# Kernel tuning notes

Measured on AMD Instinct MI355X. Metric: run time of the kernel, lower is better.

Reference implementation:

```python
import jax, jax.numpy as jnp
import numpy as np

N, S, E, H = 2, 2048, 1024, 16
D = E // H  # head_dim = 64


def setup_inputs() -> dict:
    key = jax.random.key(0)
    k1, k2, k3 = jax.random.split(key, 3)
    x = jax.random.normal(k1, (N, S, E), dtype=jnp.float32)
    # Xavier-uniform-scaled weights (torch Linear layout: [out_features, in_features])
    lim_qkv = (6.0 / (E + 3 * E)) ** 0.5
    qkv_w = jax.random.uniform(k2, (3 * E, E), dtype=jnp.float32, minval=-lim_qkv, maxval=lim_qkv)
    lim_o = (6.0 / (E + E)) ** 0.5
    o_w = jax.random.uniform(k3, (E, E), dtype=jnp.float32, minval=-lim_o, maxval=lim_o)
    # causal look-ahead mask: positions where mask == 0 are excluded
    attn_mask = jnp.tril(jnp.ones((S, S), dtype=jnp.int32))
    return {"x": x, "attn_mask": attn_mask, "qkv_w": qkv_w, "o_w": o_w}


def reference(x, attn_mask, qkv_w, o_w):
    n, s, e = x.shape
    qkv = x @ qkv_w.T                              # (N, S, 3E)
    q, k, v = jnp.split(qkv, 3, axis=-1)
    # (N, S, E) -> (N, H, S, D)
    def to_heads(t):
        return t.reshape(n, s, H, D).transpose(0, 2, 1, 3)
    q, k, v = to_heads(q), to_heads(k), to_heads(v)
    scale = 1.0 / jnp.sqrt(jnp.asarray(D, dtype=x.dtype))
    logits = jnp.einsum('bhqd,bhkd->bhqk', q, k) * scale   # (N, H, S, S)
    mask = attn_mask.reshape(1, 1, s, s)                    # expand_mask: 2D -> (1,1,S,S)
    logits = jnp.where(mask == 0, -jnp.inf, logits)
    attn_weights = jax.nn.softmax(logits, axis=-1)
    values = jnp.einsum('bhqk,bhkd->bhqd', attn_weights, v)  # (N, H, S, D)
    values = values.transpose(0, 2, 1, 3).reshape(n, s, e)
    o = values @ o_w.T
    return o
```

## Files before the change

### kernel.cpp

```cpp
#include <hip/hip_runtime.h>
#include <math.h>

typedef unsigned short u16;
typedef unsigned int uint;
typedef __attribute__((ext_vector_type(8))) short bf16x8;
typedef __attribute__((ext_vector_type(8))) _Float16 half8;
typedef __attribute__((ext_vector_type(4))) float floatx4;

__device__ __forceinline__ u16 f2bf(float f) {
  union { float f; uint u; } c; c.f = f;
  return (u16)((c.u + 0x7FFFu + ((c.u >> 16) & 1u)) >> 16);
}
__device__ __forceinline__ float bf2f(u16 h) {
  union { uint u; float f; } c; c.u = ((uint)h) << 16;
  return c.f;
}
__device__ __forceinline__ u16 h2u(_Float16 h) {
  union { _Float16 h; u16 u; } c; c.h = h;
  return c.u;
}

#if __has_builtin(__builtin_amdgcn_exp2f)
#define EX2 __builtin_amdgcn_exp2f
#else
#define EX2 exp2f
#endif

__device__ __forceinline__ void gl_lds16(const u16* g, u16* l) {
  __builtin_amdgcn_global_load_lds(
      (const __attribute__((address_space(1))) uint*)g,
      (__attribute__((address_space(3))) uint*)l, 16, 0, 0);
}

__device__ __forceinline__ void store_c(u16* p, float v) { *p = f2bf(v); }
__device__ __forceinline__ void store_c(float* p, float v) { *p = v; }

#define ROR16(x, n)                                                        \
  __builtin_bit_cast(float, __builtin_amdgcn_update_dpp(                   \
      __builtin_bit_cast(int, (x)), __builtin_bit_cast(int, (x)),          \
      0x120 + (n), 0xF, 0xF, false))
__device__ __forceinline__ float rsum16(float x) {
  x += ROR16(x, 8); x += ROR16(x, 4); x += ROR16(x, 2); x += ROR16(x, 1);
  return x;
}

__global__ __launch_bounds__(256) void cvt_all(const float* __restrict__ x,
                                               const float* __restrict__ qw,
                                               const float* __restrict__ ow,
                                               u16* __restrict__ xb,
                                               u16* __restrict__ wb,
                                               u16* __restrict__ ob) {
  int bx = blockIdx.x;
  const float* src; u16* dst; int off;
  if (bx < 2048) { src = x; dst = xb; off = bx; }
  else if (bx < 3584) { src = qw; dst = wb; off = bx - 2048; }
  else { src = ow; dst = ob; off = bx - 3584; }
  int i = (off * 256 + threadIdx.x) * 8;
  float4 a = *(const float4*)(src + i);
  float4 b = *(const float4*)(src + i + 4);
  bf16x8 r;
  r[0] = (short)f2bf(a.x); r[1] = (short)f2bf(a.y);
  r[2] = (short)f2bf(a.z); r[3] = (short)f2bf(a.w);
  r[4] = (short)f2bf(b.x); r[5] = (short)f2bf(b.y);
  r[6] = (short)f2bf(b.z); r[7] = (short)f2bf(b.w);
  *(bf16x8*)(dst + i) = r;
}

__global__ __launch_bounds__(256) void vtrans(const u16* __restrict__ qkv,
                                              u16* __restrict__ vt) {
  constexpr int S = 2048, E = 1024, TE = 3072;
  __shared__ u16 tile[64 * 72];
  const int t = threadIdx.x;
  const int kv0 = blockIdx.x * 64;
  const int bh = blockIdx.y, b = bh >> 4, h = bh & 15;
  const u16* src = qkv + (size_t)b * S * TE + 2 * E + h * 64;
#pragma unroll
  for (int i = 0; i < 2; ++i) {
    int c = t + i * 256;
    int kv = c >> 3, d0 = (c & 7) * 8;
    *(bf16x8*)&tile[kv * 72 + d0] = *(const bf16x8*)&src[(size_t)(kv0 + kv) * TE + d0];
  }
  __syncthreads();
  u16* dst = vt + (size_t)bh * 64 * S + kv0;
#pragma unroll
  for (int i = 0; i < 2; ++i) {
    int c = t + i * 256;
    int d = c >> 3, k0 = (c & 7) * 8;
    bf16x8 r;
#pragma unroll
    for (int j = 0; j < 8; ++j)
      r[j] = (short)h2u((_Float16)bf2f(tile[(k0 + j) * 72 + d]));
    *(bf16x8*)&dst[(size_t)d * S + k0] = r;
  }
}

template <typename TC>
__global__ __launch_bounds__(256) void gemm_bt(const u16* __restrict__ A,
                                               const u16* __restrict__ B,
                                               TC* __restrict__ C,
                                               int K, int N) {
  __shared__ __align__(16) u16 lds_a[128 * 64];
  __shared__ __align__(16) u16 lds_b[128 * 64];
  const int t = threadIdx.x;
  const int w = t >> 6, lane = t & 63, quad = lane >> 4, lr = lane & 15;
  const int wr = w >> 1, wc = w & 1;
  const int m0 = blockIdx.y * 128, n0 = blockIdx.x * 128;

  const int srow = lane >> 3;
  const int scol = ((lane & 7) ^ srow) * 8;
  const u16* Ab = A + (size_t)(m0 + w * 32 + srow) * K + scol;
  const u16* Bb = B + (size_t)(n0 + w * 32 + srow) * K + scol;
  u16* la = lds_a + (w * 32) * 64;
  u16* lb = lds_b + (w * 32) * 64;

  floatx4 acc[4][4];
#pragma unroll
  for (int i = 0; i < 4; ++i)
#pragma unroll
    for (int j = 0; j < 4; ++j) acc[i][j] = {0.f, 0.f, 0.f, 0.f};

  for (int k0 = 0; k0 < K; k0 += 64) {
#pragma unroll
    for (int j = 0; j < 4; ++j) {
      gl_lds16(Ab + (size_t)(j * 8) * K + k0, la + j * 8 * 64);
      gl_lds16(Bb + (size_t)(j * 8) * K + k0, lb + j * 8 * 64);
    }
    __syncthreads();
#pragma unroll
    for (int kk = 0; kk < 2; ++kk) {
      bf16x8 af[4], bfr[4];
#pragma unroll
      for (int mi = 0; mi < 4; ++mi)
        af[mi] = *(const bf16x8*)&lds_a[(wr * 64 + mi * 16 + lr) * 64 +
                                        (((kk * 4 + quad) ^ (lr & 7)) * 8)];
#pragma unroll
      for (int ni = 0; ni < 4; ++ni)
        bfr[ni] = *(const bf16x8*)&lds_b[(wc * 64 + ni * 16 + lr) * 64 +
                                         (((kk * 4 + quad) ^ (lr & 7)) * 8)];
#pragma unroll
      for (int mi = 0; mi < 4; ++mi)
#pragma unroll
        for (int ni = 0; ni < 4; ++ni)
          acc[mi][ni] = __builtin_amdgcn_mfma_f32_16x16x32_bf16(
              af[mi], bfr[ni], acc[mi][ni], 0, 0, 0);
    }
    __syncthreads();
  }
#pragma unroll
  for (int mi = 0; mi < 4; ++mi)
#pragma unroll
    for (int r = 0; r < 4; ++r) {
      int m = m0 + wr * 64 + mi * 16 + quad * 4 + r;
#pragma unroll
      for (int ni = 0; ni < 4; ++ni) {
        int n = n0 + wc * 64 + ni * 16 + lr;
        store_c(&C[(size_t)m * N + n], acc[mi][ni][r]);
      }
    }
}

template <typename TC>
__global__ __launch_bounds__(256) void gemm_bt64(const u16* __restrict__ A,
                                                 const u16* __restrict__ B,
                                                 TC* __restrict__ C,
                                                 int K, int N) {
  __shared__ __align__(16) u16 lds_a[64 * 64];
  __shared__ __align__(16) u16 lds_b[128 * 64];
  const int t = threadIdx.x;
  const int w = t >> 6, lane = t & 63, quad = lane >> 4, lr = lane & 15;
  const int m0 = blockIdx.y * 64, n0 = blockIdx.x * 128;

  const int srow = lane >> 3;
  const int scol = ((lane & 7) ^ srow) * 8;
  const u16* Ab = A + (size_t)(m0 + srow) * K + scol;
  const u16* Bb = B + (size_t)(n0 + srow) * K + scol;

  floatx4 acc[4][2];
#pragma unroll
  for (int i = 0; i < 4; ++i)
#pragma unroll
    for (int j = 0; j < 2; ++j) acc[i][j] = {0.f, 0.f, 0.f, 0.f};

  for (int k0 = 0; k0 < K; k0 += 64) {
#pragma unroll
    for (int i = 0; i < 2; ++i)
      gl_lds16(Ab + (size_t)((w * 2 + i) * 8) * K + k0, &lds_a[(w * 2 + i) * 8 * 64]);
#pragma unroll
    for (int i = 0; i < 4; ++i)
      gl_lds16(Bb + (size_t)((w * 4 + i) * 8) * K + k0, &lds_b[(w * 4 + i) * 8 * 64]);
    __syncthreads();
#pragma unroll
    for (int kk = 0; kk < 2; ++kk) {
      bf16x8 af[4], bfr[2];
#pragma unroll
      for (int mi = 0; mi < 4; ++mi)
        af[mi] = *(const bf16x8*)&lds_a[(mi * 16 + lr) * 64 +
                                        (((kk * 4 + quad) ^ (lr & 7)) * 8)];
#pragma unroll
      for (int ni = 0; ni < 2; ++ni)
        bfr[ni] = *(const bf16x8*)&lds_b[(w * 32 + ni * 16 + lr) * 64 +
                                         (((kk * 4 + quad) ^ (lr & 7)) * 8)];
#pragma unroll
      for (int mi = 0; mi < 4; ++mi)
#pragma unroll
        for (int ni = 0; ni < 2; ++ni)
          acc[mi][ni] = __builtin_amdgcn_mfma_f32_16x16x32_bf16(
              af[mi], bfr[ni], acc[mi][ni], 0, 0, 0);
    }
    __syncthreads();
  }
#pragma unroll
  for (int mi = 0; mi < 4; ++mi)
#pragma unroll
    for (int r = 0; r < 4; ++r) {
      int m = m0 + mi * 16 + quad * 4 + r;
#pragma unroll
      for (int ni = 0; ni < 2; ++ni) {
        int n = n0 + w * 32 + ni * 16 + lr;
        store_c(&C[(size_t)m * N + n], acc[mi][ni][r]);
      }
    }
}

__global__ __launch_bounds__(512, 2) void attn_fwd(const u16* __restrict__ qkv,
                                                   const u16* __restrict__ vt,
                                                   u16* __restrict__ out,
                                                   float* __restrict__ opart,
                                                   float* __restrict__ lpart) {
  constexpr int S = 2048, E = 1024, TE = 3072;
  constexpr float NEG = -1e30f;
  __shared__ __align__(16) u16 lds_k[2][128 * 64];
  __shared__ __align__(16) u16 lds_vt[2][64 * 128];
  __shared__ __align__(16) u16 lds_p[2][4][16 * 128];
  const int t = threadIdx.x;
  const int wv = t >> 6;
  const int u = wv >> 2;
  const int w = wv & 3;
  const int lane = t & 63, quad = lane >> 4, lr = lane & 15;
  const int bx = (int)blockIdx.x;
  const int h = bx & 15, pr = (bx >> 4) & 7, hB = bx >> 7;
  const int qtH = 15 - pr;
  const int b = u;
  const int bh = b * 16 + h;
  const int pid = (b * 16 + h) * 8 + pr;
  const size_t base = (size_t)b * S * TE;
  const u16* kbase = qkv + base + E + h * 64;
  const u16* vtb = vt + (size_t)bh * 64 * S;

  const int s8 = lane >> 3;
  const int kcol = ((lane & 7) ^ s8) * 8;
  const int vrow = lane >> 4;
  u16* const pb = &lds_p[u][w][0];
  u16* const lk = &lds_k[u][0];
  u16* const lv = &lds_vt[u][0];

  const int n0 = hB ? (8 - pr) : 8;
  const int niter = hB ? 9 : 8;

  const float QS = 0.125f * 1.44269504f;
  bf16x8 qf[2][2];
  float lst[2][4];
  floatx4 oacc[2][4];

  auto load_q = [&](int qt) {
#pragma unroll
    for (int rg = 0; rg < 2; ++rg)
#pragma unroll
      for (int kk = 0; kk < 2; ++kk) {
        bf16x8 q = *(const bf16x8*)&qkv[base +
            (size_t)(qt * 128 + w * 32 + rg * 16 + lr) * TE + h * 64 + kk * 32 + quad * 8];
#pragma unroll
        for (int jj = 0; jj < 8; ++jj) q[jj] = (short)f2bf(bf2f((u16)q[jj]) * QS);
        qf[rg][kk] = q;
      }
  };
  auto reset_acc = [&]() {
#pragma unroll
    for (int rg = 0; rg < 2; ++rg) {
#pragma unroll
      for (int r = 0; r < 4; ++r) lst[rg][r] = 0.f;
#pragma unroll
      for (int di = 0; di < 4; ++di) oacc[rg][di] = {0.f, 0.f, 0.f, 0.f};
    }
  };
  auto emit_partial = [&](int slot) {
    float* op = opart + ((size_t)slot * 256 + pid) * (128 * 64);
    float* lp = lpart + ((size_t)slot * 256 + pid) * 128;
#pragma unroll
    for (int rg = 0; rg < 2; ++rg)
#pragma unroll
      for (int r = 0; r < 4; ++r) {
        int row = w * 32 + rg * 16 + quad * 4 + r;
        float lt = rsum16(lst[rg][r]);
        if (lr == 0) lp[row] = lt;
#pragma unroll
        for (int di = 0; di < 4; ++di)
          op[row * 64 + di * 16 + lr] = oacc[rg][di][r];
      }
  };
  auto kv_of = [&](int it) -> int {
    if (!hB) return it;
    return (it < n0) ? (8 + it) : (it - n0);
  };

  load_q(qtH);
  reset_acc();

  {
    int nb = kv_of(0) * 128;
#pragma unroll
    for (int i = 0; i < 4; ++i) {
      int p0 = w * 8 + i * 32;
      int kv = nb + ((p0 & 15) + s8) * 8 + (p0 >> 4);
      gl_lds16(kbase + (size_t)kv * TE + kcol, &lk[p0 * 64]);
    }
#pragma unroll
    for (int i = 0; i < 4; ++i) {
      int d0 = w * 4 + i * 16;
      int d = d0 + vrow;
      int cbg = ((lane & 15) ^ (d & 15)) * 8;
      gl_lds16(vtb + (size_t)d * S + nb + cbg, &lv[d0 * 128]);
    }
  }

  for (int it = 0; it < niter; ++it) {
    const int kt = kv_of(it);
    const int qcur = (hB && it >= n0) ? pr : qtH;
    __syncthreads();

    floatx4 st[2][8];
#pragma unroll
    for (int rg = 0; rg < 2; ++rg)
#pragma unroll
      for (int ni = 0; ni < 8; ++ni) st[rg][ni] = {-4.f, -4.f, -4.f, -4.f};
#pragma unroll
    for (int kk = 0; kk < 2; ++kk) {
      bf16x8 kb[8];
#pragma unroll
      for (int ni = 0; ni < 8; ++ni)
        kb[ni] = *(const bf16x8*)&lk[(ni * 16 + lr) * 64 +
                                     (((kk * 4 + quad) ^ (lr & 7)) * 8)];
#pragma unroll
      for (int rg = 0; rg < 2; ++rg)
#pragma unroll
        for (int ni = 0; ni < 8; ++ni)
          st[rg][ni] = __builtin_amdgcn_mfma_f32_16x16x32_bf16(
              qf[rg][kk], kb[ni], st[rg][ni], 0, 0, 0);
    }

    half8 vb[4][4];
#pragma unroll
    for (int kk = 0; kk < 4; ++kk)
#pragma unroll
      for (int di = 0; di < 4; ++di)
        vb[kk][di] = *(const half8*)&lv[(di * 16 + lr) * 128 +
                                        (((kk * 4 + quad) ^ lr) << 3)];

    __syncthreads();

    if (it + 1 < niter) {
      int nb = kv_of(it + 1) * 128;
#pragma unroll
      for (int i = 0; i < 4; ++i) {
        int p0 = w * 8 + i * 32;
        int kv = nb + ((p0 & 15) + s8) * 8 + (p0 >> 4);
        gl_lds16(kbase + (size_t)kv * TE + kcol, &lk[p0 * 64]);
      }
#pragma unroll
      for (int i = 0; i < 4; ++i) {
        int d0 = w * 4 + i * 16;
        int d = d0 + vrow;
        int cbg = ((lane & 15) ^ (d & 15)) * 8;
        gl_lds16(vtb + (size_t)d * S + nb + cbg, &lv[d0 * 128]);
      }
    }

    const bool diag = (kt == qcur);
#pragma unroll
    for (int rg = 0; rg < 2; ++rg) {
#pragma unroll
      for (int r = 0; r < 4; ++r) {
        const int rw = quad * 4 + r;
        const int rloc = w * 32 + rg * 16 + rw;
        if (diag) {
#pragma unroll
          for (int ni = 0; ni < 8; ++ni)
            if (lr * 8 + ni > rloc) st[rg][ni][r] = NEG;
        }
        float pv[8];
#pragma unroll
        for (int ni = 0; ni < 8; ++ni) pv[ni] = EX2(st[rg][ni][r]);
        lst[rg][r] += ((pv[0] + pv[1]) + (pv[2] + pv[3])) +
                      ((pv[4] + pv[5]) + (pv[6] + pv[7]));
        half8 p8;
#pragma unroll
        for (int ni = 0; ni < 8; ++ni) p8[ni] = (_Float16)pv[ni];
        *(half8*)&pb[rw * 128 + (((lr + rw) & 15) << 3)] = p8;
      }
#pragma unroll
      for (int kk = 0; kk < 4; ++kk) {
        half8 pf = *(const half8*)&pb[lr * 128 +
                                      ((((kk * 4 + quad) + lr) & 15) << 3)];
#pragma unroll
        for (int di = 0; di < 4; ++di)
          oacc[rg][di] = __builtin_amdgcn_mfma_f32_16x16x32_f16(
              pf, vb[kk][di], oacc[rg][di], 0, 0, 0);
      }
    }

    if (hB && it == n0 - 1) {
      emit_partial(1);
      reset_acc();
      load_q(pr);
    }
  }

  if (!hB) {
    emit_partial(0);
  } else {
#pragma unroll
    for (int rg = 0; rg < 2; ++rg)
#pragma unroll
      for (int r = 0; r < 4; ++r) {
        int sg = pr * 128 + w * 32 + rg * 16 + quad * 4 + r;
        float inv_l = 1.f / rsum16(lst[rg][r]);
#pragma unroll
        for (int di = 0; di < 4; ++di)
          out[((size_t)(b * S + sg)) * E + h * 64 + di * 16 + lr] =
              f2bf(oacc[rg][di][r] * inv_l);
      }
  }
}

__global__ __launch_bounds__(256) void attn_combine(const float* __restrict__ opart,
                                                    const float* __restrict__ lpart,
                                                    u16* __restrict__ out) {
  constexpr int S = 2048, E = 1024;
  const int p = (int)blockIdx.x;
  const int pr = p & 7, bh = p >> 3, h = bh & 15, b = bh >> 4;
  const int q0 = (15 - pr) * 128;
  const int t = threadIdx.x;
  const int row = t >> 1, c0 = (t & 1) * 32;
  const float* o0 = opart + (size_t)p * (128 * 64) + row * 64 + c0;
  const float* o1 = o0 + (size_t)256 * 128 * 64;
  float l = lpart[p * 128 + row] + lpart[256 * 128 + p * 128 + row];
  float inv = 1.f / l;
  u16* dst = out + ((size_t)(b * S + q0 + row)) * E + h * 64 + c0;
#pragma unroll
  for (int i = 0; i < 4; ++i) {
    float4 a0 = ((const float4*)o0)[2 * i], a1 = ((const float4*)o0)[2 * i + 1];
    float4 b0 = ((const float4*)o1)[2 * i], b1 = ((const float4*)o1)[2 * i + 1];
    bf16x8 r;
    r[0] = (short)f2bf((a0.x + b0.x) * inv);
    r[1] = (short)f2bf((a0.y + b0.y) * inv);
    r[2] = (short)f2bf((a0.z + b0.z) * inv);
    r[3] = (short)f2bf((a0.w + b0.w) * inv);
    r[4] = (short)f2bf((a1.x + b1.x) * inv);
    r[5] = (short)f2bf((a1.y + b1.y) * inv);
    r[6] = (short)f2bf((a1.z + b1.z) * inv);
    r[7] = (short)f2bf((a1.w + b1.w) * inv);
    ((bf16x8*)dst)[i] = r;
  }
}

extern "C" void kernel_launch(void* const* d_in, const int* in_sizes, int n_in,
                              void* d_out, int out_size, void* d_ws, size_t ws_size,
                              hipStream_t stream) {
  constexpr int NB = 2, S = 2048, E = 1024;
  constexpr int M = NB * S;
  const float* x = (const float*)d_in[0];
  const float* qkv_w = (const float*)d_in[2];
  const float* o_w = (const float*)d_in[3];
  float* out = (float*)d_out;

  u16* qkv = (u16*)d_ws;
  u16* vt = qkv + (size_t)M * 3 * E;
  u16* xb = vt + (size_t)32 * 64 * S;
  u16* attn_o = xb;
  u16* wb = xb + (size_t)M * E;
  u16* ob = wb + (size_t)3 * E * E;
  float* opart = (float*)(ob + (size_t)E * E);
  float* lpart = opart + (size_t)2 * 256 * 128 * 64;

  cvt_all<<<4096, 256, 0, stream>>>(x, qkv_w, o_w, xb, wb, ob);
  gemm_bt<u16><<<dim3(3 * E / 128, M / 128), 256, 0, stream>>>(xb, wb, qkv, E, 3 * E);
  vtrans<<<dim3(S / 64, NB * 16), 256, 0, stream>>>(qkv, vt);
  attn_fwd<<<256, 512, 0, stream>>>(qkv, vt, attn_o, opart, lpart);
  attn_combine<<<256, 256, 0, stream>>>(opart, lpart, attn_o);
  gemm_bt64<float><<<dim3(E / 128, M / 64), 256, 0, stream>>>(attn_o, ob, out, E, E);
}
```

Before: 199.7 us.

## Split attention blocks per batch and double-buffer K/V tiles with prefetch

The attention kernel changes from 512-thread blocks that held both batches in two LDS halves to 256-thread blocks, one per batch, launched as 512 blocks. The two LDS K/V halves become a double buffer: the next tile is issued before computing on the current one, with a partial vmcnt wait plus a raw barrier in place of two __syncthreads. MFMA sections are also wrapped in s_setprio raises. The aim is to overlap global-to-LDS loads with compute and cut barrier stalls. The cost is hand-written waitcnt logic that has to match exactly how many loads are in flight.

```diff
diff --git a/kernel.cpp b/kernel.cpp
--- a/kernel.cpp
+++ b/kernel.cpp
@@ -222,7 +222,7 @@
     }
 }
 
-__global__ __launch_bounds__(512, 2) void attn_fwd(const u16* __restrict__ qkv,
+__global__ __launch_bounds__(256, 2) void attn_fwd(const u16* __restrict__ qkv,
                                                    const u16* __restrict__ vt,
                                                    u16* __restrict__ out,
                                                    float* __restrict__ opart,
@@ -231,18 +231,14 @@
   constexpr float NEG = -1e30f;
   __shared__ __align__(16) u16 lds_k[2][128 * 64];
   __shared__ __align__(16) u16 lds_vt[2][64 * 128];
-  __shared__ __align__(16) u16 lds_p[2][4][16 * 128];
+  __shared__ __align__(16) u16 lds_p[4][16 * 128];
   const int t = threadIdx.x;
-  const int wv = t >> 6;
-  const int u = wv >> 2;
-  const int w = wv & 3;
-  const int lane = t & 63, quad = lane >> 4, lr = lane & 15;
+  const int w = t >> 6, lane = t & 63, quad = lane >> 4, lr = lane & 15;
   const int bx = (int)blockIdx.x;
-  const int h = bx & 15, pr = (bx >> 4) & 7, hB = bx >> 7;
+  const int h = bx & 15, pr = (bx >> 4) & 7, hB = (bx >> 7) & 1, b = bx >> 8;
   const int qtH = 15 - pr;
-  const int b = u;
   const int bh = b * 16 + h;
-  const int pid = (b * 16 + h) * 8 + pr;
+  const int pid = bh * 8 + pr;
   const size_t base = (size_t)b * S * TE;
   const u16* kbase = qkv + base + E + h * 64;
   const u16* vtb = vt + (size_t)bh * 64 * S;
@@ -250,9 +246,7 @@
   const int s8 = lane >> 3;
   const int kcol = ((lane & 7) ^ s8) * 8;
   const int vrow = lane >> 4;
-  u16* const pb = &lds_p[u][w][0];
-  u16* const lk = &lds_k[u][0];
-  u16* const lv = &lds_vt[u][0];
+  u16* const pb = &lds_p[w][0];
 
   const int n0 = hB ? (8 - pr) : 8;
   const int niter = hB ? 9 : 8;
@@ -302,44 +296,53 @@
     if (!hB) return it;
     return (it < n0) ? (8 + it) : (it - n0);
   };
-
-  load_q(qtH);
-  reset_acc();
-
-  {
-    int nb = kv_of(0) * 128;
+  auto stage = [&](int kvt, int bi) {
+    int nb = kvt * 128;
 #pragma unroll
     for (int i = 0; i < 4; ++i) {
       int p0 = w * 8 + i * 32;
       int kv = nb + ((p0 & 15) + s8) * 8 + (p0 >> 4);
-      gl_lds16(kbase + (size_t)kv * TE + kcol, &lk[p0 * 64]);
+      gl_lds16(kbase + (size_t)kv * TE + kcol, &lds_k[bi][p0 * 64]);
     }
 #pragma unroll
     for (int i = 0; i < 4; ++i) {
       int d0 = w * 4 + i * 16;
       int d = d0 + vrow;
       int cbg = ((lane & 15) ^ (d & 15)) * 8;
-      gl_lds16(vtb + (size_t)d * S + nb + cbg, &lv[d0 * 128]);
-    }
-  }
+      gl_lds16(vtb + (size_t)d * S + nb + cbg, &lds_vt[bi][d0 * 128]);
+    }
+  };
+
+  load_q(qtH);
+  stage(kv_of(0), 0);
+  reset_acc();
 
   for (int it = 0; it < niter; ++it) {
+    const int cur = it & 1;
     const int kt = kv_of(it);
     const int qcur = (hB && it >= n0) ? pr : qtH;
-    __syncthreads();
+
+    if (it + 1 < niter) {
+      stage(kv_of(it + 1), cur ^ 1);
+      asm volatile("s_waitcnt vmcnt(8)\n\ts_barrier" ::: "memory");
+    } else {
+      asm volatile("s_waitcnt vmcnt(0)\n\ts_barrier" ::: "memory");
+    }
+    __builtin_amdgcn_sched_barrier(0);
 
     floatx4 st[2][8];
 #pragma unroll
     for (int rg = 0; rg < 2; ++rg)
 #pragma unroll
       for (int ni = 0; ni < 8; ++ni) st[rg][ni] = {-4.f, -4.f, -4.f, -4.f};
+    __builtin_amdgcn_s_setprio(1);
 #pragma unroll
     for (int kk = 0; kk < 2; ++kk) {
       bf16x8 kb[8];
 #pragma unroll
       for (int ni = 0; ni < 8; ++ni)
-        kb[ni] = *(const bf16x8*)&lk[(ni * 16 + lr) * 64 +
-                                     (((kk * 4 + quad) ^ (lr & 7)) * 8)];
+        kb[ni] = *(const bf16x8*)&lds_k[cur][(ni * 16 + lr) * 64 +
+                                            (((kk * 4 + quad) ^ (lr & 7)) * 8)];
 #pragma unroll
       for (int rg = 0; rg < 2; ++rg)
 #pragma unroll
@@ -347,33 +350,18 @@
           st[rg][ni] = __builtin_amdgcn_mfma_f32_16x16x32_bf16(
               qf[rg][kk], kb[ni], st[rg][ni], 0, 0, 0);
     }
+    __builtin_amdgcn_s_setprio(0);
 
     half8 vb[4][4];
 #pragma unroll
     for (int kk = 0; kk < 4; ++kk)
 #pragma unroll
       for (int di = 0; di < 4; ++di)
-        vb[kk][di] = *(const half8*)&lv[(di * 16 + lr) * 128 +
-                                        (((kk * 4 + quad) ^ lr) << 3)];
-
-    __syncthreads();
-
-    if (it + 1 < niter) {
-      int nb = kv_of(it + 1) * 128;
-#pragma unroll
-      for (int i = 0; i < 4; ++i) {
-        int p0 = w * 8 + i * 32;
-        int kv = nb + ((p0 & 15) + s8) * 8 + (p0 >> 4);
-        gl_lds16(kbase + (size_t)kv * TE + kcol, &lk[p0 * 64]);
-      }
-#pragma unroll
-      for (int i = 0; i < 4; ++i) {
-        int d0 = w * 4 + i * 16;
-        int d = d0 + vrow;
-        int cbg = ((lane & 15) ^ (d & 15)) * 8;
-        gl_lds16(vtb + (size_t)d * S + nb + cbg, &lv[d0 * 128]);
-      }
-    }
+        vb[kk][di] = *(const half8*)&lds_vt[cur][(di * 16 + lr) * 128 +
+                                                 (((kk * 4 + quad) ^ lr) << 3)];
+
+    asm volatile("s_waitcnt lgkmcnt(0)\n\ts_barrier" ::: "memory");
+    __builtin_amdgcn_sched_barrier(0);
 
     const bool diag = (kt == qcur);
 #pragma unroll
@@ -397,6 +385,7 @@
         for (int ni = 0; ni < 8; ++ni) p8[ni] = (_Float16)pv[ni];
         *(half8*)&pb[rw * 128 + (((lr + rw) & 15) << 3)] = p8;
       }
+      __builtin_amdgcn_s_setprio(1);
 #pragma unroll
       for (int kk = 0; kk < 4; ++kk) {
         half8 pf = *(const half8*)&pb[lr * 128 +
@@ -406,6 +395,7 @@
           oacc[rg][di] = __builtin_amdgcn_mfma_f32_16x16x32_f16(
               pf, vb[kk][di], oacc[rg][di], 0, 0, 0);
       }
+      __builtin_amdgcn_s_setprio(0);
     }
 
     if (hB && it == n0 - 1) {
@@ -485,7 +475,7 @@
   cvt_all<<<4096, 256, 0, stream>>>(x, qkv_w, o_w, xb, wb, ob);
   gemm_bt<u16><<<dim3(3 * E / 128, M / 128), 256, 0, stream>>>(xb, wb, qkv, E, 3 * E);
   vtrans<<<dim3(S / 64, NB * 16), 256, 0, stream>>>(qkv, vt);
-  attn_fwd<<<256, 512, 0, stream>>>(qkv, vt, attn_o, opart, lpart);
+  attn_fwd<<<512, 256, 0, stream>>>(qkv, vt, attn_o, opart, lpart);
   attn_combine<<<256, 256, 0, stream>>>(opart, lpart, attn_o);
   gemm_bt64<float><<<dim3(E / 128, M / 64), 256, 0, stream>>>(attn_o, ob, out, E, E);
 }
```

New measurement: 184.3 us. 7.7% less time.
